# Kernel optimization log

Measured on AMD Instinct MI355X. Metric: run time of the kernel, lower is better.

The kernel has to match this reference:

```python
import jax, jax.numpy as jnp
import numpy as np

NUM_GROUPS = 32
EPS = 1e-6


def group_norm(x, scale, bias):
    # x: [B, C, H, W]
    b, c, h, w = x.shape
    g = NUM_GROUPS
    xg = x.reshape(b, g, c // g, h, w)
    mean = xg.mean(axis=(2, 3, 4), keepdims=True)
    var = xg.var(axis=(2, 3, 4), keepdims=True)
    xg = (xg - mean) * jax.lax.rsqrt(var + EPS)
    x = xg.reshape(b, c, h, w)
    return x * scale[None, :, None, None] + bias[None, :, None, None]


def conv1x1(x, w, b):
    # x: [B, C, H, W], w: [O, C] (1x1 conv weight), b: [O]
    return jnp.einsum('oc,bchw->bohw', w, x) + b[None, :, None, None]


def setup_inputs() -> dict:
    key = jax.random.key(0)
    ks = jax.random.split(key, 6)
    B, C, H, W = 8, 512, 64, 64
    s = 1.0 / np.sqrt(C)
    return {
        'x': jax.random.normal(ks[0], (B, C, H, W), dtype=jnp.float32),
        'gn_scale': jnp.ones((C,), jnp.float32),
        'gn_bias': jnp.zeros((C,), jnp.float32),
        'wq': jax.random.normal(ks[1], (C, C), jnp.float32) * s,
        'bq': jnp.zeros((C,), jnp.float32),
        'wk': jax.random.normal(ks[2], (C, C), jnp.float32) * s,
        'bk': jnp.zeros((C,), jnp.float32),
        'wv': jax.random.normal(ks[3], (C, C), jnp.float32) * s,
        'bv': jnp.zeros((C,), jnp.float32),
        'wo': jax.random.normal(ks[4], (C, C), jnp.float32) * s,
        'bo': jnp.zeros((C,), jnp.float32),
    }


def reference(x, gn_scale, gn_bias, wq, bq, wk, bk, wv, bv, wo, bo):
    b, c, h, w = x.shape
    h_ = group_norm(x, gn_scale, gn_bias)
    q = conv1x1(h_, wq, bq).reshape(b, c, h * w)  # [B, C, N]
    k = conv1x1(h_, wk, bk).reshape(b, c, h * w)
    v = conv1x1(h_, wv, bv).reshape(b, c, h * w)
    scale = c ** (-0.5)
    # scores[b, i, j] = sum_c q[b,c,i] * k[b,c,j]
    scores = jnp.einsum('bci,bcj->bij', q, k) * scale
    attn = jax.nn.softmax(scores, axis=2)  # softmax over key positions j
    # h_[b, c, i] = sum_j v[b,c,j] * attn[b,i,j]
    out = jnp.einsum('bcj,bij->bci', v, attn).reshape(b, c, h, w)
    out = conv1x1(out, wo, bo)
    return x + out
```

## Files before the change

### kernel.cpp

```cpp
#include <hip/hip_runtime.h>

using u16 = unsigned short;
using s16x8 = __attribute__((ext_vector_type(8))) short;
using f32x4 = __attribute__((ext_vector_type(4))) float;

#define DEV static __device__ __forceinline__

DEV u16 bf16b(float f) {
  unsigned u = __builtin_bit_cast(unsigned, f);
  return (u16)((u + 0x7fffu + ((u >> 16) & 1u)) >> 16);
}

DEV void gload16(const void* g, void* l) {
  __builtin_amdgcn_global_load_lds((const __attribute__((address_space(1))) unsigned int*)g,
                                   (__attribute__((address_space(3))) unsigned int*)l, 16, 0, 0);
}

DEV f32x4 mfma16(s16x8 a, s16x8 b, f32x4 c) {
  return __builtin_amdgcn_mfma_f32_16x16x32_bf16(a, b, c, 0, 0, 0);
}

__global__ void k_cvt_w(const float* __restrict__ w0, const float* __restrict__ w1,
                        const float* __restrict__ w2, const float* __restrict__ w3,
                        u16* __restrict__ out) {
  int i = blockIdx.x * 256 + threadIdx.x;
  int which = i >> 18, off = i & 0x3ffff;
  const float* s = which == 0 ? w0 : which == 1 ? w1 : which == 2 ? w2 : w3;
  out[i] = bf16b(s[off]);
}

__global__ __launch_bounds__(1024) void k_gn(const float* __restrict__ x,
                                             const float* __restrict__ gsc,
                                             const float* __restrict__ gbi,
                                             u16* __restrict__ hT) {
  const int b = blockIdx.x >> 5, g = blockIdx.x & 31;
  const int tid = threadIdx.x;
  const float* xs = x + (size_t)(b * 512 + g * 16) * 4096;

  float s = 0.f, s2 = 0.f;
  const float4* xv = (const float4*)xs;
  #pragma unroll
  for (int kq = 0; kq < 16; kq++) {
    float4 v = xv[tid + kq * 1024];
    s  += v.x + v.y + v.z + v.w;
    s2 += v.x * v.x + v.y * v.y + v.z * v.z + v.w * v.w;
  }
  #pragma unroll
  for (int m = 1; m < 64; m <<= 1) { s += __shfl_xor(s, m, 64); s2 += __shfl_xor(s2, m, 64); }
  __shared__ float rs[16], rs2[16];
  __shared__ float stat[2];
  int wid = tid >> 6;
  if ((tid & 63) == 0) { rs[wid] = s; rs2[wid] = s2; }
  __syncthreads();
  if (tid == 0) {
    float a = 0.f, a2 = 0.f;
    for (int i = 0; i < 16; i++) { a += rs[i]; a2 += rs2[i]; }
    float mean = a * (1.f / 65536.f);
    float var = a2 * (1.f / 65536.f) - mean * mean;
    stat[0] = mean;
    stat[1] = rsqrtf(var + 1e-6f);
  }
  __syncthreads();
  const float mean = stat[0], rstd = stat[1];
  const int cc = tid & 15;
  const float aa = rstd * gsc[g * 16 + cc];
  const float bb = gbi[g * 16 + cc] - mean * aa;

  __shared__ float tile[16][257];
  u16* ho = hT + (size_t)b * 4096 * 512 + g * 16;
  for (int n0 = 0; n0 < 4096; n0 += 256) {
    __syncthreads();
    #pragma unroll
    for (int rr = 0; rr < 4; rr++) {
      int r = rr * 4 + (tid >> 8);
      tile[r][tid & 255] = xs[(size_t)r * 4096 + n0 + (tid & 255)];
    }
    __syncthreads();
    #pragma unroll
    for (int kq = 0; kq < 4; kq++) {
      int nl = ((tid >> 4) << 2) + kq;
      float v = tile[cc][nl];
      ho[(size_t)(n0 + nl) * 512 + cc] = bf16b(v * aa + bb);
    }
  }
}

template<bool BIAS_ROW, bool RESID>
DEV void gemm_nt_core(const u16* __restrict__ A, const u16* __restrict__ Bm,
                      const float* __restrict__ bias, const float* __restrict__ resid,
                      void* __restrict__ outp, int m0, int n0, int ldo) {
  __shared__ __align__(16) u16 As[128 * 64];
  __shared__ __align__(16) u16 Bs[128 * 64];
  const int tid = threadIdx.x;
  const int lane = tid & 63;
  const int w = tid >> 6;
  const int wr = w >> 1, wc = w & 1;
  f32x4 acc[4][4] = {};

  for (int kc = 0; kc < 8; kc++) {
    #pragma unroll
    for (int q = 0; q < 4; q++) {
      int idx = q * 256 + tid;
      int row = idx >> 3, sl = idx & 7;
      int koff = kc * 64 + ((sl ^ (row & 7)) << 3);
      gload16(A  + (size_t)(m0 + row) * 512 + koff, As + (q * 256 + w * 64) * 8);
      gload16(Bm + (size_t)(n0 + row) * 512 + koff, Bs + (q * 256 + w * 64) * 8);
    }
    __syncthreads();
    #pragma unroll
    for (int kk = 0; kk < 2; kk++) {
      s16x8 af[4], bfr[4];
      #pragma unroll
      for (int m = 0; m < 4; m++) {
        int row = wr * 64 + m * 16 + (lane & 15);
        int cq = kk * 4 + (lane >> 4);
        af[m] = *(const s16x8*)&As[row * 64 + ((cq ^ (row & 7)) << 3)];
      }
      #pragma unroll
      for (int n = 0; n < 4; n++) {
        int row = wc * 64 + n * 16 + (lane & 15);
        int cq = kk * 4 + (lane >> 4);
        bfr[n] = *(const s16x8*)&Bs[row * 64 + ((cq ^ (row & 7)) << 3)];
      }
      #pragma unroll
      for (int m = 0; m < 4; m++)
        #pragma unroll
        for (int n = 0; n < 4; n++)
          acc[m][n] = mfma16(af[m], bfr[n], acc[m][n]);
    }
    __syncthreads();
  }

  float bcol[4];
  if (!BIAS_ROW) {
    #pragma unroll
    for (int n = 0; n < 4; n++) bcol[n] = bias[n0 + wc * 64 + n * 16 + (lane & 15)];
  }
  #pragma unroll
  for (int m = 0; m < 4; m++) {
    #pragma unroll
    for (int r = 0; r < 4; r++) {
      int row = m0 + wr * 64 + m * 16 + ((lane >> 4) << 2) + r;
      float badd = BIAS_ROW ? bias[row] : 0.f;
      #pragma unroll
      for (int n = 0; n < 4; n++) {
        int col = n0 + wc * 64 + n * 16 + (lane & 15);
        float v = acc[m][n][r] + (BIAS_ROW ? badd : bcol[n]);
        if (RESID) {
          size_t o = (size_t)row * ldo + col;
          ((float*)outp)[o] = v + resid[o];
        } else {
          ((u16*)outp)[(size_t)row * ldo + col] = bf16b(v);
        }
      }
    }
  }
}

__global__ __launch_bounds__(256) void k_gemm_qk(const u16* __restrict__ hT,
    const u16* __restrict__ wqb, const u16* __restrict__ wkb,
    const float* __restrict__ bq, const float* __restrict__ bk,
    u16* __restrict__ qT, u16* __restrict__ kT) {
  int z = blockIdx.z, b = z >> 1;
  const u16* A = hT + (size_t)b * 4096 * 512;
  const u16* W = (z & 1) ? wkb : wqb;
  const float* bb = (z & 1) ? bk : bq;
  u16* out = ((z & 1) ? kT : qT) + (size_t)b * 4096 * 512;
  gemm_nt_core<false, false>(A, W, bb, nullptr, out, blockIdx.x * 128, blockIdx.y * 128, 512);
}

__global__ __launch_bounds__(256) void k_gemm_v(const u16* __restrict__ wvb,
    const u16* __restrict__ hT, const float* __restrict__ bv, u16* __restrict__ vS) {
  int b = blockIdx.z;
  gemm_nt_core<true, false>(wvb, hT + (size_t)b * 4096 * 512, bv, nullptr,
                            vS + (size_t)b * 512 * 4096, blockIdx.x * 128, blockIdx.y * 128, 4096);
}

__global__ __launch_bounds__(256) void k_gemm_o(const u16* __restrict__ wob,
    const u16* __restrict__ oT, const float* __restrict__ bo,
    const float* __restrict__ x, float* __restrict__ y) {
  int b = blockIdx.z;
  gemm_nt_core<true, true>(wob, oT + (size_t)b * 4096 * 512, bo,
                           x + (size_t)b * 512 * 4096,
                           y + (size_t)b * 512 * 4096, blockIdx.x * 128, blockIdx.y * 128, 4096);
}

__global__ __launch_bounds__(512) void k_attn(const u16* __restrict__ qT,
                                              const u16* __restrict__ kT,
                                              const u16* __restrict__ vS,
                                              u16* __restrict__ oT) {
  const int it = blockIdx.x, b = blockIdx.y;
  const int tid = threadIdx.x, lane = tid & 63, w = tid >> 6;
  const int rg = w >> 1, cg = w & 1;
  const u16* qp = qT + (size_t)b * 4096 * 512;
  const u16* kp = kT + (size_t)b * 4096 * 512;
  const u16* vp = vS + (size_t)b * 512 * 4096;

  __shared__ __align__(16) u16 Ks[64 * 512];
  __shared__ __align__(16) u16 Vs[2][512 * 32];
  __shared__ __align__(16) u16 Ps[64 * 64];
  __shared__ float l_lds[2][64];

  s16x8 qf[16];
  {
    const u16* qrow = qp + (size_t)(it * 64 + rg * 16 + (lane & 15)) * 512 + ((lane >> 4) << 3);
    #pragma unroll
    for (int t = 0; t < 16; t++) qf[t] = *(const s16x8*)(qrow + t * 32);
  }
  f32x4 oacc[16] = {};
  float lpart[4] = {0.f, 0.f, 0.f, 0.f};

  #pragma unroll
  for (int q = 0; q < 8; q++) {
    int idx = q * 512 + tid;
    int j = idx >> 6, sl = idx & 63;
    gload16(kp + (size_t)j * 512 + ((sl ^ (j & 7)) << 3), Ks + (q * 512 + w * 64) * 8);
  }
  #pragma unroll
  for (int q = 0; q < 4; q++) {
    int idx = q * 512 + tid;
    int c = idx >> 2, sl = idx & 3;
    gload16(vp + (size_t)c * 4096 + ((sl ^ (c & 3)) << 3), Vs[0] + (q * 512 + w * 64) * 8);
  }
  __syncthreads();

  const float se = 0.044194173824159216f;

  for (int jt = 0; jt < 64; jt++) {
    f32x4 sacc[2] = {};
    #pragma unroll
    for (int t = 0; t < 16; t++) {
      #pragma unroll
      for (int nf = 0; nf < 2; nf++) {
        int j = cg * 32 + nf * 16 + (lane & 15);
        int cq = t * 4 + (lane >> 4);
        s16x8 bfrag = *(const s16x8*)&Ks[j * 512 + ((cq ^ (j & 7)) << 3)];
        sacc[nf] = mfma16(qf[t], bfrag, sacc[nf]);
      }
    }
    #pragma unroll
    for (int nf = 0; nf < 2; nf++) {
      int jcol = cg * 32 + nf * 16 + (lane & 15);
      #pragma unroll
      for (int r = 0; r < 4; r++) {
        float p = __expf(sacc[nf][r] * se);
        lpart[r] += p;
        int grow = rg * 16 + ((lane >> 4) << 2) + r;
        int off = (grow * 128 + jcol * 2) ^ ((grow & 7) << 4);
        *(u16*)((char*)Ps + off) = bf16b(p);
      }
    }
    __syncthreads();

    if (jt < 63) {
      #pragma unroll
      for (int q = 0; q < 8; q++) {
        int idx = q * 512 + tid;
        int j = idx >> 6, sl = idx & 63;
        gload16(kp + (size_t)(jt * 64 + 64 + j) * 512 + ((sl ^ (j & 7)) << 3),
                Ks + (q * 512 + w * 64) * 8);
      }
    }
    #pragma unroll
    for (int q = 0; q < 4; q++) {
      int idx = q * 512 + tid;
      int c = idx >> 2, sl = idx & 3;
      gload16(vp + (size_t)c * 4096 + jt * 64 + 32 + ((sl ^ (c & 3)) << 3),
              Vs[1] + (q * 512 + w * 64) * 8);
    }
    {
      int prow = rg * 16 + (lane & 15);
      int poff = (prow * 128 + ((lane >> 4) << 4)) ^ ((prow & 7) << 4);
      s16x8 pf = *(const s16x8*)((char*)Ps + poff);
      #pragma unroll
      for (int nf = 0; nf < 16; nf++) {
        int c = cg * 256 + nf * 16 + (lane & 15);
        int sl = (lane >> 4) ^ (c & 3);
        s16x8 vf = *(const s16x8*)&Vs[0][c * 32 + sl * 8];
        oacc[nf] = mfma16(pf, vf, oacc[nf]);
      }
    }
    __syncthreads();

    if (jt < 63) {
      #pragma unroll
      for (int q = 0; q < 4; q++) {
        int idx = q * 512 + tid;
        int c = idx >> 2, sl = idx & 3;
        gload16(vp + (size_t)c * 4096 + (jt + 1) * 64 + ((sl ^ (c & 3)) << 3),
                Vs[0] + (q * 512 + w * 64) * 8);
      }
    }
    {
      int prow = rg * 16 + (lane & 15);
      int poff = (prow * 128 + 64 + ((lane >> 4) << 4)) ^ ((prow & 7) << 4);
      s16x8 pf = *(const s16x8*)((char*)Ps + poff);
      #pragma unroll
      for (int nf = 0; nf < 16; nf++) {
        int c = cg * 256 + nf * 16 + (lane & 15);
        int sl = (lane >> 4) ^ (c & 3);
        s16x8 vf = *(const s16x8*)&Vs[1][c * 32 + sl * 8];
        oacc[nf] = mfma16(pf, vf, oacc[nf]);
      }
    }
    __syncthreads();
  }

  #pragma unroll
  for (int r = 0; r < 4; r++) {
    float lv = lpart[r];
    lv += __shfl_xor(lv, 1, 64);
    lv += __shfl_xor(lv, 2, 64);
    lv += __shfl_xor(lv, 4, 64);
    lv += __shfl_xor(lv, 8, 64);
    if ((lane & 15) == 0) l_lds[cg][rg * 16 + ((lane >> 4) << 2) + r] = lv;
  }
  __syncthreads();
  float linv[4];
  #pragma unroll
  for (int r = 0; r < 4; r++) {
    int grow = rg * 16 + ((lane >> 4) << 2) + r;
    linv[r] = 1.0f / (l_lds[0][grow] + l_lds[1][grow]);
  }
  u16* op = oT + ((size_t)b * 4096 + it * 64) * 512;
  #pragma unroll
  for (int nf = 0; nf < 16; nf++) {
    int col = cg * 256 + nf * 16 + (lane & 15);
    #pragma unroll
    for (int r = 0; r < 4; r++) {
      int grow = rg * 16 + ((lane >> 4) << 2) + r;
      op[(size_t)grow * 512 + col] = bf16b(oacc[nf][r] * linv[r]);
    }
  }
}

extern "C" void kernel_launch(void* const* d_in, const int* in_sizes, int n_in,
                              void* d_out, int out_size, void* d_ws, size_t ws_size,
                              hipStream_t stream) {
  const float* x   = (const float*)d_in[0];
  const float* gsc = (const float*)d_in[1];
  const float* gbi = (const float*)d_in[2];
  const float* wq  = (const float*)d_in[3];
  const float* bq  = (const float*)d_in[4];
  const float* wk  = (const float*)d_in[5];
  const float* bk  = (const float*)d_in[6];
  const float* wv  = (const float*)d_in[7];
  const float* bv  = (const float*)d_in[8];
  const float* wo  = (const float*)d_in[9];
  const float* bo  = (const float*)d_in[10];
  float* out = (float*)d_out;
  char* ws = (char*)d_ws;

  u16* hT = (u16*)ws;
  u16* vS = (u16*)(ws + ((size_t)32 << 20));
  u16* wB = (u16*)(ws + ((size_t)64 << 20));
  u16* wqb = wB;
  u16* wkb = wB + 262144;
  u16* wvb = wB + 2 * 262144;
  u16* wob = wB + 3 * 262144;
  u16* qT = (u16*)d_out;
  u16* kT = qT + (size_t)8 * 4096 * 512;

  k_cvt_w<<<4096, 256, 0, stream>>>(wq, wk, wv, wo, wB);
  k_gn<<<256, 1024, 0, stream>>>(x, gsc, gbi, hT);
  k_gemm_qk<<<dim3(32, 4, 16), 256, 0, stream>>>(hT, wqb, wkb, bq, bk, qT, kT);
  k_gemm_v<<<dim3(4, 32, 8), 256, 0, stream>>>(wvb, hT, bv, vS);
  k_attn<<<dim3(64, 8), 512, 0, stream>>>(qT, kT, vS, hT );
  k_gemm_o<<<dim3(4, 32, 8), 256, 0, stream>>>(wob, hT, bo, x, out);
}
```

Before: 765.0 us.

## Restructure attention to 32-key tiles with double-buffered K and 32x32 MFMA for PV

The attention kernel now walks keys in 32-wide tiles with double-buffered K and V in LDS. The next tile's K is prefetched before the score MFMAs, replacing the single 64-row K buffer that was reloaded between barriers. The PV product switches from 16x16x32 to 32x32x16 MFMA with a new 2x4 wave tiling, which cuts LDS fragment reads per FLOP. This doubles the loop trip count and the number of barriers per key, and it changes the V swizzle and the output register layout.

```diff
diff --git a/kernel.cpp b/kernel.cpp
--- a/kernel.cpp
+++ b/kernel.cpp
@@ -3,6 +3,7 @@
 using u16 = unsigned short;
 using s16x8 = __attribute__((ext_vector_type(8))) short;
 using f32x4 = __attribute__((ext_vector_type(4))) float;
+using f32x16 = __attribute__((ext_vector_type(16))) float;
 
 #define DEV static __device__ __forceinline__
 
@@ -18,6 +19,9 @@
 
 DEV f32x4 mfma16(s16x8 a, s16x8 b, f32x4 c) {
   return __builtin_amdgcn_mfma_f32_16x16x32_bf16(a, b, c, 0, 0, 0);
+}
+DEV f32x16 mfma32(s16x8 a, s16x8 b, f32x16 c) {
+  return __builtin_amdgcn_mfma_f32_32x32x16_bf16(a, b, c, 0, 0, 0);
 }
 
 __global__ void k_cvt_w(const float* __restrict__ w0, const float* __restrict__ w1,
@@ -192,13 +196,15 @@
   const int it = blockIdx.x, b = blockIdx.y;
   const int tid = threadIdx.x, lane = tid & 63, w = tid >> 6;
   const int rg = w >> 1, cg = w & 1;
+  const int rg2 = w >> 2, cg2 = w & 3;
+
   const u16* qp = qT + (size_t)b * 4096 * 512;
   const u16* kp = kT + (size_t)b * 4096 * 512;
   const u16* vp = vS + (size_t)b * 512 * 4096;
 
-  __shared__ __align__(16) u16 Ks[64 * 512];
+  __shared__ __align__(16) u16 Ks[2][32 * 512];
   __shared__ __align__(16) u16 Vs[2][512 * 32];
-  __shared__ __align__(16) u16 Ps[64 * 64];
+  __shared__ __align__(16) u16 Ps[64 * 32];
   __shared__ float l_lds[2][64];
 
   s16x8 qf[16];
@@ -207,100 +213,77 @@
     #pragma unroll
     for (int t = 0; t < 16; t++) qf[t] = *(const s16x8*)(qrow + t * 32);
   }
-  f32x4 oacc[16] = {};
+  f32x16 oacc[4] = {};
   float lpart[4] = {0.f, 0.f, 0.f, 0.f};
 
-  #pragma unroll
-  for (int q = 0; q < 8; q++) {
-    int idx = q * 512 + tid;
-    int j = idx >> 6, sl = idx & 63;
-    gload16(kp + (size_t)j * 512 + ((sl ^ (j & 7)) << 3), Ks + (q * 512 + w * 64) * 8);
-  }
+  const int wbase = w * 64 * 8;
+
   #pragma unroll
   for (int q = 0; q < 4; q++) {
-    int idx = q * 512 + tid;
-    int c = idx >> 2, sl = idx & 3;
-    gload16(vp + (size_t)c * 4096 + ((sl ^ (c & 3)) << 3), Vs[0] + (q * 512 + w * 64) * 8);
+    int d = q * 512 + tid, j = d >> 6, p = d & 63;
+    gload16(kp + (size_t)j * 512 + ((p ^ (j & 7)) << 3), Ks[0] + q * 4096 + wbase);
+  }
+  #pragma unroll
+  for (int q = 0; q < 4; q++) {
+    int d = q * 512 + tid, c = d >> 2, p = d & 3;
+    gload16(vp + (size_t)c * 4096 + ((p ^ ((c >> 1) & 3)) << 3), Vs[0] + q * 4096 + wbase);
   }
   __syncthreads();
 
   const float se = 0.044194173824159216f;
-
-  for (int jt = 0; jt < 64; jt++) {
-    f32x4 sacc[2] = {};
-    #pragma unroll
-    for (int t = 0; t < 16; t++) {
-      #pragma unroll
-      for (int nf = 0; nf < 2; nf++) {
-        int j = cg * 32 + nf * 16 + (lane & 15);
-        int cq = t * 4 + (lane >> 4);
-        s16x8 bfrag = *(const s16x8*)&Ks[j * 512 + ((cq ^ (j & 7)) << 3)];
-        sacc[nf] = mfma16(qf[t], bfrag, sacc[nf]);
-      }
-    }
-    #pragma unroll
-    for (int nf = 0; nf < 2; nf++) {
-      int jcol = cg * 32 + nf * 16 + (lane & 15);
+  const int jS = cg * 16 + (lane & 15);
+  const int xmS = (jS & 7) << 3;
+  const int irow = rg2 * 32 + (lane & 31);
+  const int sband = lane >> 5;
+
+  for (int jt = 0; jt < 128; jt++) {
+    const int cur = jt & 1, nxt = cur ^ 1;
+    if (jt < 127) {
+      const u16* kn = kp + (size_t)(jt + 1) * 32 * 512;
+      #pragma unroll
+      for (int q = 0; q < 4; q++) {
+        int d = q * 512 + tid, j = d >> 6, p = d & 63;
+        gload16(kn + (size_t)j * 512 + ((p ^ (j & 7)) << 3), Ks[nxt] + q * 4096 + wbase);
+      }
+    }
+    {
+      f32x4 sacc = {};
+      const u16* kb = Ks[cur] + jS * 512;
+      #pragma unroll
+      for (int t = 0; t < 16; t++) {
+        int off = (((t * 4 + (lane >> 4)) << 3)) ^ xmS;
+        sacc = mfma16(qf[t], *(const s16x8*)(kb + off), sacc);
+      }
       #pragma unroll
       for (int r = 0; r < 4; r++) {
-        float p = __expf(sacc[nf][r] * se);
-        lpart[r] += p;
+        float pv = __expf(sacc[r] * se);
+        lpart[r] += pv;
         int grow = rg * 16 + ((lane >> 4) << 2) + r;
-        int off = (grow * 128 + jcol * 2) ^ ((grow & 7) << 4);
-        *(u16*)((char*)Ps + off) = bf16b(p);
-      }
-    }
-    __syncthreads();
-
-    if (jt < 63) {
-      #pragma unroll
-      for (int q = 0; q < 8; q++) {
-        int idx = q * 512 + tid;
-        int j = idx >> 6, sl = idx & 63;
-        gload16(kp + (size_t)(jt * 64 + 64 + j) * 512 + ((sl ^ (j & 7)) << 3),
-                Ks + (q * 512 + w * 64) * 8);
-      }
-    }
-    #pragma unroll
-    for (int q = 0; q < 4; q++) {
-      int idx = q * 512 + tid;
-      int c = idx >> 2, sl = idx & 3;
-      gload16(vp + (size_t)c * 4096 + jt * 64 + 32 + ((sl ^ (c & 3)) << 3),
-              Vs[1] + (q * 512 + w * 64) * 8);
-    }
-    {
-      int prow = rg * 16 + (lane & 15);
-      int poff = (prow * 128 + ((lane >> 4) << 4)) ^ ((prow & 7) << 4);
-      s16x8 pf = *(const s16x8*)((char*)Ps + poff);
-      #pragma unroll
-      for (int nf = 0; nf < 16; nf++) {
-        int c = cg * 256 + nf * 16 + (lane & 15);
-        int sl = (lane >> 4) ^ (c & 3);
-        s16x8 vf = *(const s16x8*)&Vs[0][c * 32 + sl * 8];
-        oacc[nf] = mfma16(pf, vf, oacc[nf]);
-      }
-    }
-    __syncthreads();
-
-    if (jt < 63) {
+        int psl = ((jS >> 3) ^ ((grow >> 1) & 3)) & 3;
+        Ps[grow * 32 + psl * 8 + (jS & 7)] = bf16b(pv);
+      }
+    }
+    __syncthreads();
+
+    if (jt < 127) {
+      const u16* vn = vp + (size_t)(jt + 1) * 32;
       #pragma unroll
       for (int q = 0; q < 4; q++) {
-        int idx = q * 512 + tid;
-        int c = idx >> 2, sl = idx & 3;
-        gload16(vp + (size_t)c * 4096 + (jt + 1) * 64 + ((sl ^ (c & 3)) << 3),
-                Vs[0] + (q * 512 + w * 64) * 8);
-      }
-    }
-    {
-      int prow = rg * 16 + (lane & 15);
-      int poff = (prow * 128 + 64 + ((lane >> 4) << 4)) ^ ((prow & 7) << 4);
-      s16x8 pf = *(const s16x8*)((char*)Ps + poff);
-      #pragma unroll
-      for (int nf = 0; nf < 16; nf++) {
-        int c = cg * 256 + nf * 16 + (lane & 15);
-        int sl = (lane >> 4) ^ (c & 3);
-        s16x8 vf = *(const s16x8*)&Vs[1][c * 32 + sl * 8];
-        oacc[nf] = mfma16(pf, vf, oacc[nf]);
+        int d = q * 512 + tid, c = d >> 2, p = d & 3;
+        gload16(vn + (size_t)c * 4096 + ((p ^ ((c >> 1) & 3)) << 3), Vs[nxt] + q * 4096 + wbase);
+      }
+    }
+    #pragma unroll
+    for (int ks = 0; ks < 2; ks++) {
+      int s = ks * 2 + sband;
+      int pp = (s ^ ((irow >> 1) & 3)) & 3;
+      s16x8 pf = *(const s16x8*)(Ps + irow * 32 + pp * 8);
+      #pragma unroll
+      for (int n = 0; n < 4; n++) {
+        int c = cg2 * 128 + n * 32 + (lane & 31);
+        int vpp = (s ^ ((c >> 1) & 3)) & 3;
+        s16x8 vf = *(const s16x8*)(Vs[cur] + c * 32 + vpp * 8);
+        oacc[n] = mfma32(pf, vf, oacc[n]);
       }
     }
     __syncthreads();
@@ -316,20 +299,21 @@
     if ((lane & 15) == 0) l_lds[cg][rg * 16 + ((lane >> 4) << 2) + r] = lv;
   }
   __syncthreads();
-  float linv[4];
-  #pragma unroll
-  for (int r = 0; r < 4; r++) {
-    int grow = rg * 16 + ((lane >> 4) << 2) + r;
-    linv[r] = 1.0f / (l_lds[0][grow] + l_lds[1][grow]);
+
+  float linv[16];
+  #pragma unroll
+  for (int e = 0; e < 16; e++) {
+    int i = rg2 * 32 + (e & 3) + 8 * (e >> 2) + 4 * sband;
+    linv[e] = 1.0f / (l_lds[0][i] + l_lds[1][i]);
   }
   u16* op = oT + ((size_t)b * 4096 + it * 64) * 512;
   #pragma unroll
-  for (int nf = 0; nf < 16; nf++) {
-    int col = cg * 256 + nf * 16 + (lane & 15);
-    #pragma unroll
-    for (int r = 0; r < 4; r++) {
-      int grow = rg * 16 + ((lane >> 4) << 2) + r;
-      op[(size_t)grow * 512 + col] = bf16b(oacc[nf][r] * linv[r]);
+  for (int n = 0; n < 4; n++) {
+    int col = cg2 * 128 + n * 32 + (lane & 31);
+    #pragma unroll
+    for (int e = 0; e < 16; e++) {
+      int i = rg2 * 32 + (e & 3) + 8 * (e >> 2) + 4 * sband;
+      op[(size_t)i * 512 + col] = bf16b(oacc[n][e] * linv[e]);
     }
   }
 }
```

Measured after the change: 754.6 us. Within noise of the previous version (-1.4%).
